# Optimization experiments

Measured on AMD Instinct MI355X. Metric: run time of the kernel, lower is better.

The kernel has to match this reference:

```python
import jax, jax.numpy as jnp
import numpy as np

VOCABSIZE = 100000
EMBEDSIZE = 128
BATCH = 262144


def setup_inputs() -> dict:
    key = jax.random.key(0)
    k1, k2, k3, k4, k5 = jax.random.split(key, 5)
    xs = jax.random.randint(k1, (BATCH,), 0, VOCABSIZE, dtype=jnp.int64 if jax.config.jax_enable_x64 else jnp.int32)
    ys = jax.random.randint(k2, (BATCH,), 0, VOCABSIZE, dtype=jnp.int64 if jax.config.jax_enable_x64 else jnp.int32)
    metric = jax.random.normal(k3, (EMBEDSIZE, EMBEDSIZE), dtype=jnp.float32)
    EMBEDM = jax.random.normal(k4, (VOCABSIZE, EMBEDSIZE), dtype=jnp.float32)
    # Original inits NEGEMBEDM to zeros; we use small random values so the
    # output / gradients are non-degenerate for kernel correctness testing.
    NEGEMBEDM = jax.random.normal(k5, (VOCABSIZE, EMBEDSIZE), dtype=jnp.float32) * 0.1
    return {"xs": xs, "ys": ys, "metric": metric, "EMBEDM": EMBEDM, "NEGEMBEDM": NEGEMBEDM}


def reference(xs, ys, metric, EMBEDM, NEGEMBEDM):
    # Faithful math: diag((E[xs] @ metric) @ N[ys].T) == sum((E[xs] @ metric) * N[ys], -1).
    # We compute the batched bilinear form directly, avoiding the O(B^2*D)
    # full matmul + diag extraction of the original.
    xsembeds = EMBEDM[xs]          # [B, D]
    ysembeds = NEGEMBEDM[ys]       # [B, D]
    d = jnp.einsum('bd,de,be->b', xsembeds, metric, ysembeds)  # [B]
    return jax.nn.sigmoid(2.0 * d - 1.0)
```

## Files before the change

### kernel.cpp

```cpp
#include <hip/hip_runtime.h>
#include <hip/hip_fp16.h>

#define D      128
#define NROWS  100000
#define RB     64
#define NE     ((NROWS + RB - 1) / RB)

typedef __attribute__((ext_vector_type(8))) _Float16 f16x8;
typedef __attribute__((ext_vector_type(2))) _Float16 f16x2;
typedef __attribute__((ext_vector_type(4))) float    f32x4;

union F16x8U { _Float16 h[8]; f16x8 v; };
union F32x4U { float f[4]; f32x4 v; };

typedef __attribute__((address_space(1))) const void gvoid;
typedef __attribute__((address_space(3))) void       lvoid;

__global__ __launch_bounds__(256) void convert_M16(
    const float* __restrict__ M,
    _Float16* __restrict__ mh, _Float16* __restrict__ ml)
{
    const int q    = blockIdx.x * 256 + threadIdx.x;
    const int kk   = q >> 9;
    const int cf   = (q >> 6) & 7;
    const int lane = q & 63;
    const int col  = cf * 16 + (lane & 15);
    const int k0   = kk * 32 + (lane >> 4) * 8;

    F16x8U h, l;
    #pragma unroll
    for (int j = 0; j < 8; ++j) {
        float f = M[(k0 + j) * D + col];
        _Float16 hh = (_Float16)f;
        h.h[j] = hh;
        l.h[j] = (_Float16)(f - (float)hh);
    }
    *(f16x8*)(mh + q * 8) = h.v;
    *(f16x8*)(ml + q * 8) = l.v;
}

__global__ __launch_bounds__(256, 3) void gemm_E(
    const float* __restrict__ E,
    const _Float16* __restrict__ mh, const _Float16* __restrict__ ml,
    _Float16* __restrict__ Ep)
{
    __shared__ float lds[RB * D];

    const int tid  = threadIdx.x;
    const int lane = tid & 63;
    const int w    = tid >> 6;
    const int rb   = (int)blockIdx.x * RB;
    const int lrow = lane & 15;
    const int lk   = lane >> 4;

    f16x8 bh[4][2], bl[4][2];
    #pragma unroll
    for (int kk = 0; kk < 4; ++kk)
        #pragma unroll
        for (int cfl = 0; cfl < 2; ++cfl) {
            const int off = ((kk * 8 + w * 2 + cfl) * 64 + lane) * 8;
            bh[kk][cfl] = *(const f16x8*)(mh + off);
            bl[kk][cfl] = *(const f16x8*)(ml + off);
        }

    #pragma unroll
    for (int i = 0; i < 8; ++i) {
        const int S  = w * 512 + i * 64 + lane;
        const int r  = S >> 5;
        const int u  = (S & 31) ^ (r & 15);
        const int gr = min(rb + r, NROWS - 1);
        const float* src = E + (size_t)gr * D + u * 4;
        __builtin_amdgcn_global_load_lds(
            (gvoid*)src, (lvoid*)&lds[(w * 512 + i * 64) * 4], 16, 0, 0);
    }

    f32x4 acc[4][2];
    #pragma unroll
    for (int rf = 0; rf < 4; ++rf)
        #pragma unroll
        for (int cfl = 0; cfl < 2; ++cfl)
            acc[rf][cfl] = (f32x4){0.f, 0.f, 0.f, 0.f};

    asm volatile("s_waitcnt vmcnt(0)" ::: "memory");
    __syncthreads();
    __builtin_amdgcn_sched_barrier(0);

    #pragma unroll
    for (int kk = 0; kk < 4; ++kk)
        #pragma unroll
        for (int cfl = 0; cfl < 2; ++cfl)
            asm volatile("" : "+v"(bh[kk][cfl]), "+v"(bl[kk][cfl]));

    #pragma unroll
    for (int kk = 0; kk < 4; ++kk) {
        F16x8U a16[4];
        #pragma unroll
        for (int rf = 0; rf < 4; ++rf) {
            const int r  = rf * 16 + lrow;
            const int t0 = kk * 8 + lk * 2;
            F32x4U x, y;
            x.v = *(const f32x4*)&lds[(r * 32 + ((t0    ) ^ (r & 15))) * 4];
            y.v = *(const f32x4*)&lds[(r * 32 + ((t0 + 1) ^ (r & 15))) * 4];
            #pragma unroll
            for (int j = 0; j < 4; ++j) {
                a16[rf].h[j]     = (_Float16)x.f[j];
                a16[rf].h[j + 4] = (_Float16)y.f[j];
            }
        }

        #pragma unroll
        for (int rf = 0; rf < 4; ++rf)
            #pragma unroll
            for (int cfl = 0; cfl < 2; ++cfl) {
                acc[rf][cfl] = __builtin_amdgcn_mfma_f32_16x16x32_f16(
                    a16[rf].v, bh[kk][cfl], acc[rf][cfl], 0, 0, 0);
                acc[rf][cfl] = __builtin_amdgcn_mfma_f32_16x16x32_f16(
                    a16[rf].v, bl[kk][cfl], acc[rf][cfl], 0, 0, 0);
            }
    }

    #pragma unroll
    for (int rf = 0; rf < 4; ++rf)
        #pragma unroll
        for (int i = 0; i < 4; ++i) {
            const int row = rb + rf * 16 + lk * 4 + i;
            if (row < NROWS) {
                f16x2 o;
                o[0] = (_Float16)acc[rf][0][i];
                o[1] = (_Float16)acc[rf][1][i];
                *(f16x2*)(Ep + (size_t)row * D + lrow * 8 + w * 2) = o;
            }
        }
}

__global__ __launch_bounds__(256) void gather_dotN(
    const int* __restrict__ xs, const int* __restrict__ ys,
    const _Float16* __restrict__ Ep, const float* __restrict__ N,
    float* __restrict__ out)
{
    const int tid = threadIdx.x;
    const int o0  = blockIdx.x * 32 + (tid >> 4) * 2;
    const int l   = tid & 15;

    const int x0 = xs[o0], x1 = xs[o0 + 1];
    const int y0 = ys[o0], y1 = ys[o0 + 1];

    const f16x8 a0 = *(const f16x8*)(Ep + (size_t)x0 * D + l * 8);
    const f16x8 a1 = *(const f16x8*)(Ep + (size_t)x1 * D + l * 8);
    const float* n0 = N + (size_t)y0 * D + l;
    const float* n1 = N + (size_t)y1 * D + l;

    float r0 = 0.f, r1 = 0.f;
    #pragma unroll
    for (int j = 0; j < 8; ++j) {
        r0 += (float)a0[j] * n0[16 * j];
        r1 += (float)a1[j] * n1[16 * j];
    }

    r0 += __shfl_xor(r0, 1); r1 += __shfl_xor(r1, 1);
    r0 += __shfl_xor(r0, 2); r1 += __shfl_xor(r1, 2);
    r0 += __shfl_xor(r0, 4); r1 += __shfl_xor(r1, 4);
    r0 += __shfl_xor(r0, 8); r1 += __shfl_xor(r1, 8);

    if (l == 0) {
        float2 v;
        v.x = 1.0f / (1.0f + __expf(1.0f - 2.0f * r0));
        v.y = 1.0f / (1.0f + __expf(1.0f - 2.0f * r1));
        *(float2*)(out + o0) = v;
    }
}

extern "C" void kernel_launch(void* const* d_in, const int* in_sizes, int n_in,
                              void* d_out, int out_size, void* d_ws, size_t ws_size,
                              hipStream_t stream) {
    const int*   xs     = (const int*)d_in[0];
    const int*   ys     = (const int*)d_in[1];
    const float* metric = (const float*)d_in[2];
    const float* EMBEDM = (const float*)d_in[3];
    const float* NEGEM  = (const float*)d_in[4];
    float*       out    = (float*)d_out;

    const int B = in_sizes[0];

    char* ws = (char*)d_ws;
    _Float16* Ep = (_Float16*)ws;
    _Float16* mh = (_Float16*)(ws + (64u << 20));
    _Float16* ml = (_Float16*)(ws + (64u << 20) + (64u << 10));

    convert_M16<<<8, 256, 0, stream>>>(metric, mh, ml);

    gemm_E<<<NE, 256, 0, stream>>>(EMBEDM, mh, ml, Ep);

    gather_dotN<<<B / 32, 256, 0, stream>>>(xs, ys, Ep, NEGEM, out);
}
```

Measured before the change: 56.88 us.

## Make E-projection GEMM persistent with double-buffered LDS prefetch

New measurement: 56.48 us. Within noise of the previous version (-0.7%).

```diff
diff --git a/kernel.cpp b/kernel.cpp
--- a/kernel.cpp
+++ b/kernel.cpp
@@ -4,7 +4,8 @@
 #define D      128
 #define NROWS  100000
 #define RB     64
-#define NE     ((NROWS + RB - 1) / RB)
+#define NTILES ((NROWS + RB - 1) / RB)
+#define GRID_E 512
 
 typedef __attribute__((ext_vector_type(8))) _Float16 f16x8;
 typedef __attribute__((ext_vector_type(2))) _Float16 f16x2;
@@ -39,30 +40,9 @@
     *(f16x8*)(ml + q * 8) = l.v;
 }
 
-__global__ __launch_bounds__(256, 3) void gemm_E(
-    const float* __restrict__ E,
-    const _Float16* __restrict__ mh, const _Float16* __restrict__ ml,
-    _Float16* __restrict__ Ep)
-{
-    __shared__ float lds[RB * D];
-
-    const int tid  = threadIdx.x;
-    const int lane = tid & 63;
-    const int w    = tid >> 6;
-    const int rb   = (int)blockIdx.x * RB;
-    const int lrow = lane & 15;
-    const int lk   = lane >> 4;
-
-    f16x8 bh[4][2], bl[4][2];
-    #pragma unroll
-    for (int kk = 0; kk < 4; ++kk)
-        #pragma unroll
-        for (int cfl = 0; cfl < 2; ++cfl) {
-            const int off = ((kk * 8 + w * 2 + cfl) * 64 + lane) * 8;
-            bh[kk][cfl] = *(const f16x8*)(mh + off);
-            bl[kk][cfl] = *(const f16x8*)(ml + off);
-        }
-
+__device__ __forceinline__ void stage_tile(
+    const float* __restrict__ E, float* Lbase, int rb, int w, int lane)
+{
     #pragma unroll
     for (int i = 0; i < 8; ++i) {
         const int S  = w * 512 + i * 64 + lane;
@@ -71,19 +51,37 @@
         const int gr = min(rb + r, NROWS - 1);
         const float* src = E + (size_t)gr * D + u * 4;
         __builtin_amdgcn_global_load_lds(
-            (gvoid*)src, (lvoid*)&lds[(w * 512 + i * 64) * 4], 16, 0, 0);
-    }
-
-    f32x4 acc[4][2];
-    #pragma unroll
-    for (int rf = 0; rf < 4; ++rf)
-        #pragma unroll
-        for (int cfl = 0; cfl < 2; ++cfl)
-            acc[rf][cfl] = (f32x4){0.f, 0.f, 0.f, 0.f};
-
+            (gvoid*)src, (lvoid*)(Lbase + (w * 512 + i * 64) * 4), 16, 0, 0);
+    }
+}
+
+__global__ __launch_bounds__(256, 2) void gemm_E(
+    const float* __restrict__ E,
+    const _Float16* __restrict__ mh, const _Float16* __restrict__ ml,
+    _Float16* __restrict__ Ep)
+{
+    __shared__ float lds[2][RB * D];
+
+    const int tid  = threadIdx.x;
+    const int lane = tid & 63;
+    const int w    = tid >> 6;
+    const int lrow = lane & 15;
+    const int lk   = lane >> 4;
+
+    f16x8 bh[4][2], bl[4][2];
+    #pragma unroll
+    for (int kk = 0; kk < 4; ++kk)
+        #pragma unroll
+        for (int cfl = 0; cfl < 2; ++cfl) {
+            const int off = ((kk * 8 + w * 2 + cfl) * 64 + lane) * 8;
+            bh[kk][cfl] = *(const f16x8*)(mh + off);
+            bl[kk][cfl] = *(const f16x8*)(ml + off);
+        }
+
+    const int t0 = (int)blockIdx.x;
+    stage_tile(E, &lds[0][0], t0 * RB, w, lane);
     asm volatile("s_waitcnt vmcnt(0)" ::: "memory");
     __syncthreads();
-    __builtin_amdgcn_sched_barrier(0);
 
     #pragma unroll
     for (int kk = 0; kk < 4; ++kk)
@@ -91,46 +89,67 @@
         for (int cfl = 0; cfl < 2; ++cfl)
             asm volatile("" : "+v"(bh[kk][cfl]), "+v"(bl[kk][cfl]));
 
-    #pragma unroll
-    for (int kk = 0; kk < 4; ++kk) {
-        F16x8U a16[4];
-        #pragma unroll
-        for (int rf = 0; rf < 4; ++rf) {
-            const int r  = rf * 16 + lrow;
-            const int t0 = kk * 8 + lk * 2;
-            F32x4U x, y;
-            x.v = *(const f32x4*)&lds[(r * 32 + ((t0    ) ^ (r & 15))) * 4];
-            y.v = *(const f32x4*)&lds[(r * 32 + ((t0 + 1) ^ (r & 15))) * 4];
-            #pragma unroll
-            for (int j = 0; j < 4; ++j) {
-                a16[rf].h[j]     = (_Float16)x.f[j];
-                a16[rf].h[j + 4] = (_Float16)y.f[j];
+    int cur = 0;
+    for (int t = t0; t < NTILES; t += GRID_E) {
+        const int tn = t + GRID_E;
+        if (tn < NTILES) stage_tile(E, &lds[cur ^ 1][0], tn * RB, w, lane);
+
+        const float* L = &lds[cur][0];
+        f32x4 acc[4][2];
+        #pragma unroll
+        for (int rf = 0; rf < 4; ++rf)
+            #pragma unroll
+            for (int cfl = 0; cfl < 2; ++cfl)
+                acc[rf][cfl] = (f32x4){0.f, 0.f, 0.f, 0.f};
+
+        #pragma unroll
+        for (int kk = 0; kk < 4; ++kk) {
+            F16x8U a16[4];
+            #pragma unroll
+            for (int rf = 0; rf < 4; ++rf) {
+                const int r  = rf * 16 + lrow;
+                const int q0 = kk * 8 + lk * 2;
+                F32x4U x, y;
+                x.v = *(const f32x4*)&L[(r * 32 + ((q0    ) ^ (r & 15))) * 4];
+                y.v = *(const f32x4*)&L[(r * 32 + ((q0 + 1) ^ (r & 15))) * 4];
+                #pragma unroll
+                for (int j = 0; j < 4; ++j) {
+                    a16[rf].h[j]     = (_Float16)x.f[j];
+                    a16[rf].h[j + 4] = (_Float16)y.f[j];
+                }
             }
+            #pragma unroll
+            for (int rf = 0; rf < 4; ++rf)
+                #pragma unroll
+                for (int cfl = 0; cfl < 2; ++cfl) {
+                    acc[rf][cfl] = __builtin_amdgcn_mfma_f32_16x16x32_f16(
+                        a16[rf].v, bh[kk][cfl], acc[rf][cfl], 0, 0, 0);
+                    acc[rf][cfl] = __builtin_amdgcn_mfma_f32_16x16x32_f16(
+                        a16[rf].v, bl[kk][cfl], acc[rf][cfl], 0, 0, 0);
+                }
         }
 
+        if (tn < NTILES) {
+            asm volatile("s_waitcnt vmcnt(0)" ::: "memory");
+            __syncthreads();
+        }
+
+        const int rb = t * RB;
         #pragma unroll
         for (int rf = 0; rf < 4; ++rf)
             #pragma unroll
-            for (int cfl = 0; cfl < 2; ++cfl) {
-                acc[rf][cfl] = __builtin_amdgcn_mfma_f32_16x16x32_f16(
-                    a16[rf].v, bh[kk][cfl], acc[rf][cfl], 0, 0, 0);
-                acc[rf][cfl] = __builtin_amdgcn_mfma_f32_16x16x32_f16(
-                    a16[rf].v, bl[kk][cfl], acc[rf][cfl], 0, 0, 0);
+            for (int i = 0; i < 4; ++i) {
+                const int row = rb + rf * 16 + lk * 4 + i;
+                if (row < NROWS) {
+                    f16x2 o;
+                    o[0] = (_Float16)acc[rf][0][i];
+                    o[1] = (_Float16)acc[rf][1][i];
+                    *(f16x2*)(Ep + (size_t)row * D + lrow * 8 + w * 2) = o;
+                }
             }
-    }
-
-    #pragma unroll
-    for (int rf = 0; rf < 4; ++rf)
-        #pragma unroll
-        for (int i = 0; i < 4; ++i) {
-            const int row = rb + rf * 16 + lk * 4 + i;
-            if (row < NROWS) {
-                f16x2 o;
-                o[0] = (_Float16)acc[rf][0][i];
-                o[1] = (_Float16)acc[rf][1][i];
-                *(f16x2*)(Ep + (size_t)row * D + lrow * 8 + w * 2) = o;
-            }
-        }
+
+        cur ^= 1;
+    }
 }
 
 __global__ __launch_bounds__(256) void gather_dotN(
@@ -189,7 +208,7 @@
 
     convert_M16<<<8, 256, 0, stream>>>(metric, mh, ml);
 
-    gemm_E<<<NE, 256, 0, stream>>>(EMBEDM, mh, ml, Ep);
+    gemm_E<<<GRID_E, 256, 0, stream>>>(EMBEDM, mh, ml, Ep);
 
     gather_dotN<<<B / 32, 256, 0, stream>>>(xs, ys, Ep, NEGEM, out);
 }
```

## Persistent streaming E-projection GEMM with LDS-resident metric and wider gather

Applied to the files above, without the earlier changes.

Measured after the change: 71.32 us. 25.4% more time.

```diff
diff --git a/kernel.cpp b/kernel.cpp
--- a/kernel.cpp
+++ b/kernel.cpp
@@ -1,13 +1,12 @@
 #include <hip/hip_runtime.h>
 #include <hip/hip_fp16.h>
 
-#define D      128
-#define NROWS  100000
-#define RB     64
-#define NE     ((NROWS + RB - 1) / RB)
+#define D       128
+#define NROWS   100000
+#define NTILES  (NROWS / 16)
+#define GRID_E  512
 
 typedef __attribute__((ext_vector_type(8))) _Float16 f16x8;
-typedef __attribute__((ext_vector_type(2))) _Float16 f16x2;
 typedef __attribute__((ext_vector_type(4))) float    f32x4;
 
 union F16x8U { _Float16 h[8]; f16x8 v; };
@@ -17,8 +16,7 @@
 typedef __attribute__((address_space(3))) void       lvoid;
 
 __global__ __launch_bounds__(256) void convert_M16(
-    const float* __restrict__ M,
-    _Float16* __restrict__ mh, _Float16* __restrict__ ml)
+    const float* __restrict__ M, _Float16* __restrict__ mfrag)
 {
     const int q    = blockIdx.x * 256 + threadIdx.x;
     const int kk   = q >> 9;
@@ -35,102 +33,80 @@
         h.h[j] = hh;
         l.h[j] = (_Float16)(f - (float)hh);
     }
-    *(f16x8*)(mh + q * 8) = h.v;
-    *(f16x8*)(ml + q * 8) = l.v;
+    *(f16x8*)(mfrag + q * 8)             = h.v;
+    *(f16x8*)(mfrag + (2048 + q) * 8)    = l.v;
 }
 
-__global__ __launch_bounds__(256, 3) void gemm_E(
-    const float* __restrict__ E,
-    const _Float16* __restrict__ mh, const _Float16* __restrict__ ml,
+__global__ __launch_bounds__(256, 2) void gemm_E_stream(
+    const float* __restrict__ E, const _Float16* __restrict__ mfrag,
     _Float16* __restrict__ Ep)
 {
-    __shared__ float lds[RB * D];
+    __shared__ _Float16 sm[4096 * 8];
 
     const int tid  = threadIdx.x;
     const int lane = tid & 63;
     const int w    = tid >> 6;
-    const int rb   = (int)blockIdx.x * RB;
     const int lrow = lane & 15;
     const int lk   = lane >> 4;
 
-    f16x8 bh[4][2], bl[4][2];
     #pragma unroll
-    for (int kk = 0; kk < 4; ++kk)
+    for (int it = 0; it < 16; ++it) {
+        const int slot = it * 256 + w * 64 + lane;
+        __builtin_amdgcn_global_load_lds(
+            (gvoid*)(mfrag + slot * 8), (lvoid*)(sm + (it * 256 + w * 64) * 8),
+            16, 0, 0);
+    }
+    asm volatile("s_waitcnt vmcnt(0)" ::: "memory");
+    __syncthreads();
+
+    const f16x8* Bh = (const f16x8*)sm;
+    const f16x8* Bl = (const f16x8*)sm + 2048;
+
+    const int wgid = (int)blockIdx.x * 4 + w;
+
+    for (int tb = wgid; tb < NTILES; tb += GRID_E * 4) {
+        const int row = tb * 16 + lrow;
+
+        f32x4 ax[4], ay[4];
         #pragma unroll
-        for (int cfl = 0; cfl < 2; ++cfl) {
-            const int off = ((kk * 8 + w * 2 + cfl) * 64 + lane) * 8;
-            bh[kk][cfl] = *(const f16x8*)(mh + off);
-            bl[kk][cfl] = *(const f16x8*)(ml + off);
+        for (int kk = 0; kk < 4; ++kk) {
+            const float* p = E + (size_t)row * D + kk * 32 + lk * 8;
+            ax[kk] = *(const f32x4*)p;
+            ay[kk] = *(const f32x4*)(p + 4);
         }
 
-    #pragma unroll
-    for (int i = 0; i < 8; ++i) {
-        const int S  = w * 512 + i * 64 + lane;
-        const int r  = S >> 5;
-        const int u  = (S & 31) ^ (r & 15);
-        const int gr = min(rb + r, NROWS - 1);
-        const float* src = E + (size_t)gr * D + u * 4;
-        __builtin_amdgcn_global_load_lds(
-            (gvoid*)src, (lvoid*)&lds[(w * 512 + i * 64) * 4], 16, 0, 0);
-    }
+        f32x4 acc[8];
+        #pragma unroll
+        for (int cf = 0; cf < 8; ++cf) acc[cf] = (f32x4){0.f, 0.f, 0.f, 0.f};
 
-    f32x4 acc[4][2];
-    #pragma unroll
-    for (int rf = 0; rf < 4; ++rf)
         #pragma unroll
-        for (int cfl = 0; cfl < 2; ++cfl)
-            acc[rf][cfl] = (f32x4){0.f, 0.f, 0.f, 0.f};
-
-    asm volatile("s_waitcnt vmcnt(0)" ::: "memory");
-    __syncthreads();
-    __builtin_amdgcn_sched_barrier(0);
-
-    #pragma unroll
-    for (int kk = 0; kk < 4; ++kk)
-        #pragma unroll
-        for (int cfl = 0; cfl < 2; ++cfl)
-            asm volatile("" : "+v"(bh[kk][cfl]), "+v"(bl[kk][cfl]));
-
-    #pragma unroll
-    for (int kk = 0; kk < 4; ++kk) {
-        F16x8U a16[4];
-        #pragma unroll
-        for (int rf = 0; rf < 4; ++rf) {
-            const int r  = rf * 16 + lrow;
-            const int t0 = kk * 8 + lk * 2;
-            F32x4U x, y;
-            x.v = *(const f32x4*)&lds[(r * 32 + ((t0    ) ^ (r & 15))) * 4];
-            y.v = *(const f32x4*)&lds[(r * 32 + ((t0 + 1) ^ (r & 15))) * 4];
+        for (int kk = 0; kk < 4; ++kk) {
+            F16x8U a16;
+            F32x4U x, y; x.v = ax[kk]; y.v = ay[kk];
             #pragma unroll
             for (int j = 0; j < 4; ++j) {
-                a16[rf].h[j]     = (_Float16)x.f[j];
-                a16[rf].h[j + 4] = (_Float16)y.f[j];
+                a16.h[j]     = (_Float16)x.f[j];
+                a16.h[j + 4] = (_Float16)y.f[j];
+            }
+            #pragma unroll
+            for (int cf = 0; cf < 8; ++cf) {
+                const int q = kk * 8 + cf;
+                acc[cf] = __builtin_amdgcn_mfma_f32_16x16x32_f16(
+                    a16.v, Bh[q * 64 + lane], acc[cf], 0, 0, 0);
+                acc[cf] = __builtin_amdgcn_mfma_f32_16x16x32_f16(
+                    a16.v, Bl[q * 64 + lane], acc[cf], 0, 0, 0);
             }
         }
 
         #pragma unroll
-        for (int rf = 0; rf < 4; ++rf)
+        for (int i = 0; i < 4; ++i) {
+            const int ro = tb * 16 + lk * 4 + i;
+            F16x8U o;
             #pragma unroll
-            for (int cfl = 0; cfl < 2; ++cfl) {
-                acc[rf][cfl] = __builtin_amdgcn_mfma_f32_16x16x32_f16(
-                    a16[rf].v, bh[kk][cfl], acc[rf][cfl], 0, 0, 0);
-                acc[rf][cfl] = __builtin_amdgcn_mfma_f32_16x16x32_f16(
-                    a16[rf].v, bl[kk][cfl], acc[rf][cfl], 0, 0, 0);
-            }
+            for (int cf = 0; cf < 8; ++cf) o.h[cf] = (_Float16)acc[cf][i];
+            *(f16x8*)(Ep + (size_t)ro * D + lrow * 8) = o.v;
+        }
     }
-
-    #pragma unroll
-    for (int rf = 0; rf < 4; ++rf)
-        #pragma unroll
-        for (int i = 0; i < 4; ++i) {
-            const int row = rb + rf * 16 + lk * 4 + i;
-            if (row < NROWS) {
-                f16x2 o;
-                o[0] = (_Float16)acc[rf][0][i];
-                o[1] = (_Float16)acc[rf][1][i];
-                *(f16x2*)(Ep + (size_t)row * D + lrow * 8 + w * 2) = o;
-            }
-        }
 }
 
 __global__ __launch_bounds__(256) void gather_dotN(
@@ -139,34 +115,40 @@
     float* __restrict__ out)
 {
     const int tid = threadIdx.x;
-    const int o0  = blockIdx.x * 32 + (tid >> 4) * 2;
+    const int o0  = blockIdx.x * 64 + (tid >> 4) * 4;
     const int l   = tid & 15;
 
-    const int x0 = xs[o0], x1 = xs[o0 + 1];
-    const int y0 = ys[o0], y1 = ys[o0 + 1];
+    const int4 x4 = *(const int4*)(xs + o0);
+    const int4 y4 = *(const int4*)(ys + o0);
+    const int xv[4] = {x4.x, x4.y, x4.z, x4.w};
+    const int yv[4] = {y4.x, y4.y, y4.z, y4.w};
 
-    const f16x8 a0 = *(const f16x8*)(Ep + (size_t)x0 * D + l * 8);
-    const f16x8 a1 = *(const f16x8*)(Ep + (size_t)x1 * D + l * 8);
-    const float* n0 = N + (size_t)y0 * D + l;
-    const float* n1 = N + (size_t)y1 * D + l;
-
-    float r0 = 0.f, r1 = 0.f;
+    float r[4];
     #pragma unroll
-    for (int j = 0; j < 8; ++j) {
-        r0 += (float)a0[j] * n0[16 * j];
-        r1 += (float)a1[j] * n1[16 * j];
+    for (int q = 0; q < 4; ++q) {
+        const f16x8 a = *(const f16x8*)(Ep + (size_t)xv[q] * D + l * 8);
+        const float* n = N + (size_t)yv[q] * D + l;
+        float s = 0.f;
+        #pragma unroll
+        for (int j = 0; j < 8; ++j) s += (float)a[j] * n[16 * j];
+        r[q] = s;
     }
 
-    r0 += __shfl_xor(r0, 1); r1 += __shfl_xor(r1, 1);
-    r0 += __shfl_xor(r0, 2); r1 += __shfl_xor(r1, 2);
-    r0 += __shfl_xor(r0, 4); r1 += __shfl_xor(r1, 4);
-    r0 += __shfl_xor(r0, 8); r1 += __shfl_xor(r1, 8);
+    #pragma unroll
+    for (int q = 0; q < 4; ++q) {
+        r[q] += __shfl_xor(r[q], 1);
+        r[q] += __shfl_xor(r[q], 2);
+        r[q] += __shfl_xor(r[q], 4);
+        r[q] += __shfl_xor(r[q], 8);
+    }
 
     if (l == 0) {
-        float2 v;
-        v.x = 1.0f / (1.0f + __expf(1.0f - 2.0f * r0));
-        v.y = 1.0f / (1.0f + __expf(1.0f - 2.0f * r1));
-        *(float2*)(out + o0) = v;
+        float4 v;
+        v.x = 1.0f / (1.0f + __expf(1.0f - 2.0f * r[0]));
+        v.y = 1.0f / (1.0f + __expf(1.0f - 2.0f * r[1]));
+        v.z = 1.0f / (1.0f + __expf(1.0f - 2.0f * r[2]));
+        v.w = 1.0f / (1.0f + __expf(1.0f - 2.0f * r[3]));
+        *(float4*)(out + o0) = v;
     }
 }
 
@@ -183,13 +165,12 @@
     const int B = in_sizes[0];
 
     char* ws = (char*)d_ws;
-    _Float16* Ep = (_Float16*)ws;
-    _Float16* mh = (_Float16*)(ws + (64u << 20));
-    _Float16* ml = (_Float16*)(ws + (64u << 20) + (64u << 10));
+    _Float16* Ep    = (_Float16*)ws;
+    _Float16* mfrag = (_Float16*)(ws + (64u << 20));
 
-    convert_M16<<<8, 256, 0, stream>>>(metric, mh, ml);
+    convert_M16<<<8, 256, 0, stream>>>(metric, mfrag);
 
-    gemm_E<<<NE, 256, 0, stream>>>(EMBEDM, mh, ml, Ep);
+    gemm_E_stream<<<GRID_E, 256, 0, stream>>>(EMBEDM, mfrag, Ep);
 
-    gather_dotN<<<B / 32, 256, 0, stream>>>(xs, ys, Ep, NEGEM, out);
+    gather_dotN<<<B / 64, 256, 0, stream>>>(xs, ys, Ep, NEGEM, out);
 }
```
